# Performance work log

Hardware: AMD Instinct MI355X
Metric: run time of the kernel (lower is better)

Reference implementation:

```python
import jax, jax.numpy as jnp
import numpy as np

B, S, DM = 2, 2048, 1024
H, HD = 16, 64          # n_heads, head_dim
TPF = 128               # tokens_per_frame
NF = S // TPF           # n_frames
EPS = 1e-6
ROPE_THETA = 10000.0
NEG = -1e30  # stand-in for -inf that stays finite under softmax


def setup_inputs() -> dict:
    key = jax.random.key(0)
    ks = jax.random.split(key, 3)
    x = jax.random.normal(ks[0], (B, S, DM), dtype=jnp.float32)
    Wqkv = jax.random.normal(ks[1], (3 * DM, DM), dtype=jnp.float32) * (DM ** -0.5)
    bqkv = jnp.zeros((3 * DM,), dtype=jnp.float32)
    Wout = jax.random.normal(ks[2], (DM, DM), dtype=jnp.float32) * (DM ** -0.5)
    bout = jnp.zeros((DM,), dtype=jnp.float32)
    q_scale = jnp.ones((HD,), dtype=jnp.float32)
    k_scale = jnp.ones((HD,), dtype=jnp.float32)
    return {"x": x, "Wqkv": Wqkv, "bqkv": bqkv, "q_scale": q_scale,
            "k_scale": k_scale, "Wout": Wout, "bout": bout}


def _block_causal_mask(dtype):
    # Frame-block causal: query in frame i may attend keys in frames <= i.
    # Quirk from source: rows of the LAST frame additionally mask frame 0.
    fr = jnp.arange(S) // TPF
    allowed = fr[None, :] <= fr[:, None]
    quirk = (fr[:, None] == NF - 1) & (fr[None, :] == 0)
    allowed = allowed & ~quirk
    return jnp.where(allowed, jnp.zeros((), dtype), jnp.full((), NEG, dtype))


def _rmsnorm(t, scale):
    return t * jax.lax.rsqrt(jnp.mean(t * t, axis=-1, keepdims=True) + EPS) * scale


def _rope(t):
    # half-split rotary over flat token index; t: [B,H,S,D]
    pos = jnp.arange(S, dtype=jnp.float32)
    inv_freq = 1.0 / (ROPE_THETA ** (jnp.arange(0, HD, 2, dtype=jnp.float32) / HD))
    ang = pos[:, None] * inv_freq[None, :]              # [S, D/2]
    cos = jnp.concatenate([jnp.cos(ang), jnp.cos(ang)], axis=-1)  # [S, D]
    sin = jnp.concatenate([jnp.sin(ang), jnp.sin(ang)], axis=-1)
    t1, t2 = jnp.split(t, 2, axis=-1)
    rot = jnp.concatenate([-t2, t1], axis=-1)
    return t * cos + rot * sin


def reference(x, Wqkv, bqkv, q_scale, k_scale, Wout, bout):
    qkv = x @ Wqkv.T + bqkv                        # [B,S,3*DM]
    qkv = qkv.reshape(B, S, 3, H, HD)
    q, k, v = jnp.moveaxis(qkv, 2, 0)              # each [B,S,H,D]
    q = jnp.transpose(q, (0, 2, 1, 3))             # [B,H,S,D]
    k = jnp.transpose(k, (0, 2, 1, 3))
    v = jnp.transpose(v, (0, 2, 1, 3))
    q = _rmsnorm(q, q_scale)
    k = _rmsnorm(k, k_scale)
    q = _rope(q)
    k = _rope(k)
    mask = _block_causal_mask(x.dtype)             # [S,S]
    scores = jnp.einsum('bhqd,bhkd->bhqk', q, k) * (HD ** -0.5) + mask
    attn = jax.nn.softmax(scores, axis=-1)
    o = jnp.einsum('bhqk,bhkd->bhqd', attn, v)     # [B,H,S,D]
    o = jnp.transpose(o, (0, 2, 1, 3)).reshape(B, S, DM)
    return o @ Wout.T + bout
```

## Files before the change

kernel.cpp:

```cpp
#include <hip/hip_runtime.h>
#include <cstddef>
#include <cstdint>

constexpr int CB  = 2;
constexpr int CS  = 2048;
constexpr int CDM = 1024;
constexpr int CH  = 16;
constexpr int CHD = 64;
constexpr int CTPF = 128;
constexpr int CNF = 16;

typedef __attribute__((ext_vector_type(8))) short short8;
typedef __attribute__((ext_vector_type(4))) float f32x4;

__device__ inline ushort f32_bf16_rne(float x) {
  uint32_t u = __float_as_uint(x);
  u += 0x7FFFu + ((u >> 16) & 1u);
  return (ushort)(u >> 16);
}
__device__ inline float bf16_f32(ushort h) {
  return __uint_as_float(((uint32_t)h) << 16);
}
__device__ inline void split8(const float* v, short8& H, short8& L) {
#pragma unroll
  for (int j = 0; j < 8; ++j) {
    const ushort hh = f32_bf16_rne(v[j]);
    H[j] = (short)hh;
    L[j] = (short)f32_bf16_rne(v[j] - bf16_f32(hh));
  }
}

__global__ __launch_bounds__(256) void split3(
    const float* __restrict__ s0, ushort* __restrict__ h0,
    ushort* __restrict__ l0, int n0,
    const float* __restrict__ s1, ushort* __restrict__ h1,
    ushort* __restrict__ l1, int n1,
    const float* __restrict__ s2, ushort* __restrict__ h2,
    ushort* __restrict__ l2, int n2) {
  const int ntot = n0 + n1 + n2;
  int i = blockIdx.x * 256 + threadIdx.x;
  const int stride = gridDim.x * 256;
  for (; i < ntot; i += stride) {
    const float* src;
    ushort *h, *l;
    int j = i;
    if (j < n0) {
      src = s0; h = h0; l = l0;
    } else if ((j -= n0) < n1) {
      src = s1; h = h1; l = l1;
    } else {
      j -= n1; src = s2; h = h2; l = l2;
    }
    float v[8];
    *(float4*)&v[0] = ((const float4*)src)[2 * j];
    *(float4*)&v[4] = ((const float4*)src)[2 * j + 1];
    short8 H, L;
    split8(v, H, L);
    *(short8*)&h[(size_t)j * 8] = H;
    *(short8*)&l[(size_t)j * 8] = L;
  }
}

__global__ __launch_bounds__(256) void gemm_ps(
    const ushort* __restrict__ Ah, const ushort* __restrict__ Al,
    const ushort* __restrict__ Bh, const ushort* __restrict__ Bl,
    const float* __restrict__ bias, float* __restrict__ C,
    int M, int N, int K) {
  __shared__ ushort As_h[128 * 32], As_l[128 * 32];
  __shared__ ushort Bs_h[128 * 32], Bs_l[128 * 32];
  const int tid = threadIdx.x;
  const int bm = blockIdx.y * 128;
  const int bn = blockIdx.x * 128;
  const int wid = tid >> 6;
  const int lane = tid & 63;
  const int wm = wid >> 1;
  const int wn = wid & 1;
  const int l15 = lane & 15;
  const int lk = lane >> 4;
  const int srow = tid >> 2;
  const int kq = (tid & 3) * 8;

  f32x4 acc[4][4];
#pragma unroll
  for (int i = 0; i < 4; ++i)
#pragma unroll
    for (int j = 0; j < 4; ++j) acc[i][j] = (f32x4){0.f, 0.f, 0.f, 0.f};

  for (int k0 = 0; k0 < K; k0 += 32) {
    __syncthreads();
#pragma unroll
    for (int c = 0; c < 2; ++c) {
      const int row = srow + c * 64;
      const int kg = kq ^ ((row & 6) << 2);
      const size_t ga = (size_t)(bm + row) * K + k0 + kg;
      const size_t gb = (size_t)(bn + row) * K + k0 + kg;
      const int lo = tid * 8 + c * 2048;
      __builtin_amdgcn_global_load_lds(
          (const __attribute__((address_space(1))) void*)(Ah + ga),
          (__attribute__((address_space(3))) void*)&As_h[lo], 16, 0, 0);
      __builtin_amdgcn_global_load_lds(
          (const __attribute__((address_space(1))) void*)(Al + ga),
          (__attribute__((address_space(3))) void*)&As_l[lo], 16, 0, 0);
      __builtin_amdgcn_global_load_lds(
          (const __attribute__((address_space(1))) void*)(Bh + gb),
          (__attribute__((address_space(3))) void*)&Bs_h[lo], 16, 0, 0);
      __builtin_amdgcn_global_load_lds(
          (const __attribute__((address_space(1))) void*)(Bl + gb),
          (__attribute__((address_space(3))) void*)&Bs_l[lo], 16, 0, 0);
    }
    __syncthreads();

    short8 ah[4], al[4], bh[4], bl[4];
#pragma unroll
    for (int fI = 0; fI < 4; ++fI) {
      const int ar = wm * 64 + fI * 16 + l15;
      const int aoff = ar * 32 + ((lk * 8) ^ ((ar & 6) << 2));
      ah[fI] = *(const short8*)&As_h[aoff];
      al[fI] = *(const short8*)&As_l[aoff];
      const int br = wn * 64 + fI * 16 + l15;
      const int boff = br * 32 + ((lk * 8) ^ ((br & 6) << 2));
      bh[fI] = *(const short8*)&Bs_h[boff];
      bl[fI] = *(const short8*)&Bs_l[boff];
    }
#pragma unroll
    for (int mf = 0; mf < 4; ++mf)
#pragma unroll
      for (int nf = 0; nf < 4; ++nf) {
        acc[mf][nf] = __builtin_amdgcn_mfma_f32_16x16x32_bf16(
            ah[mf], bh[nf], acc[mf][nf], 0, 0, 0);
        acc[mf][nf] = __builtin_amdgcn_mfma_f32_16x16x32_bf16(
            ah[mf], bl[nf], acc[mf][nf], 0, 0, 0);
        acc[mf][nf] = __builtin_amdgcn_mfma_f32_16x16x32_bf16(
            al[mf], bh[nf], acc[mf][nf], 0, 0, 0);
      }
  }

#pragma unroll
  for (int mf = 0; mf < 4; ++mf)
#pragma unroll
    for (int nf = 0; nf < 4; ++nf) {
      const int col = bn + wn * 64 + nf * 16 + l15;
      const int row0 = bm + wm * 64 + mf * 16 + lk * 4;
      const float bc = bias[col];
#pragma unroll
      for (int i = 0; i < 4; ++i)
        C[(size_t)(row0 + i) * N + col] = acc[mf][nf][i] + bc;
    }
}

__global__ __launch_bounds__(256) void qkv_prep(
    const float* __restrict__ qkv, const float* __restrict__ q_scale,
    const float* __restrict__ k_scale,
    ushort* __restrict__ Qh, ushort* __restrict__ Ql,
    ushort* __restrict__ Kh, ushort* __restrict__ Kl,
    ushort* __restrict__ Vth, ushort* __restrict__ Vtl) {
  __shared__ float Vtile[64][68];
  const int lane = threadIdx.x & 63;
  const int w = threadIdx.x >> 6;
  const int st = blockIdx.x;
  const int h = blockIdx.y;
  const int b = blockIdx.z;

  const float qs = q_scale[lane];
  const float ks = k_scale[lane];
  const int j = lane & 31;
  const float inv = powf(10000.0f, -(float)j * (1.0f / 32.0f));
  const float sgn = (lane < 32) ? -1.f : 1.f;

  for (int it = 0; it < 16; ++it) {
    const int sl = w * 16 + it;
    const int s = st * 64 + sl;
    const size_t row =
        ((size_t)(b * CS + s)) * (3 * CDM) + (size_t)h * CHD + lane;
    float qv = qkv[row];
    float kv = qkv[row + CDM];
    const float vv = qkv[row + 2 * CDM];

    float sq = qv * qv, sk2 = kv * kv;
#pragma unroll
    for (int off = 32; off > 0; off >>= 1) {
      sq += __shfl_xor(sq, off);
      sk2 += __shfl_xor(sk2, off);
    }
    qv *= rsqrtf(sq * (1.f / CHD) + 1e-6f) * qs;
    kv *= rsqrtf(sk2 * (1.f / CHD) + 1e-6f) * ks;

    const float ang = (float)s * inv;
    const float cs = cosf(ang);
    const float sn = sinf(ang);
    const float qp = __shfl_xor(qv, 32);
    const float kp = __shfl_xor(kv, 32);
    const float qr = fmaf(qv, cs, sgn * qp * sn) * 0.125f;
    const float kr = fmaf(kv, cs, sgn * kp * sn);

    const size_t ob = (((size_t)(b * CH + h)) * CS + s) * CHD + lane;
    const ushort qhh = f32_bf16_rne(qr);
    Qh[ob] = qhh;
    Ql[ob] = f32_bf16_rne(qr - bf16_f32(qhh));
    const ushort khh = f32_bf16_rne(kr);
    Kh[ob] = khh;
    Kl[ob] = f32_bf16_rne(kr - bf16_f32(khh));
    Vtile[lane][sl] = vv;
  }
  __syncthreads();
  const int d = threadIdx.x >> 2;
  const int sq4 = (threadIdx.x & 3) * 16;
  const size_t vb = (((size_t)(b * CH + h)) * CHD + d) * CS + st * 64 + sq4;
#pragma unroll
  for (int j0 = 0; j0 < 16; j0 += 8) {
    float v8[8];
#pragma unroll
    for (int jj = 0; jj < 8; ++jj) v8[jj] = Vtile[d][sq4 + j0 + jj];
    short8 H, L;
    split8(v8, H, L);
    *(short8*)&Vth[vb + j0] = H;
    *(short8*)&Vtl[vb + j0] = L;
  }
}

__global__ __launch_bounds__(256, 2) void attn_fwd_mfma(
    const ushort* __restrict__ Qh, const ushort* __restrict__ Ql,
    const ushort* __restrict__ Kh, const ushort* __restrict__ Kl,
    const ushort* __restrict__ Vth, const ushort* __restrict__ Vtl,
    ushort* __restrict__ Oh, ushort* __restrict__ Ol) {
  __shared__ ushort Ks_h[64 * 64], Ks_l[64 * 64];
  __shared__ ushort Vs_h[64 * 64], Vs_l[64 * 64];
  __shared__ ushort Ps_h[128 * 64], Ps_l[128 * 64];
  const int tid = threadIdx.x;
  const int b = blockIdx.x;
  const int h = blockIdx.y;
  const int fsel = blockIdx.z;
  const int f = (fsel < 8) ? (15 - fsel) : (fsel - 8);
  const int lane = tid & 63;
  const int wid = tid >> 6;
  const int l15 = lane & 15;
  const int lk = lane >> 4;
  const int qb = wid * 32;
  const size_t hb = ((size_t)(b * CH + h)) * CS * CHD;
  const size_t vtb = ((size_t)(b * CH + h)) * CHD * CS;

  short8 qh[2][2], ql[2][2];
#pragma unroll
  for (int nf = 0; nf < 2; ++nf)
#pragma unroll
    for (int ks = 0; ks < 2; ++ks) {
      const size_t qoff = hb +
          (size_t)(f * CTPF + qb + nf * 16 + l15) * CHD + ks * 32 + lk * 8;
      qh[nf][ks] = *(const short8*)(Qh + qoff);
      ql[nf][ks] = *(const short8*)(Ql + qoff);
    }

  f32x4 accO[2][4];
#pragma unroll
  for (int mo = 0; mo < 2; ++mo)
#pragma unroll
    for (int no = 0; no < 4; ++no) accO[mo][no] = (f32x4){0.f, 0.f, 0.f, 0.f};
  float m[2] = {-1e30f, -1e30f};
  float lsum[2] = {0.f, 0.f};

  const int kf0 = (f == CNF - 1) ? 1 : 0;
  for (int kf = kf0; kf <= f; ++kf) {
#pragma unroll 1
    for (int half = 0; half < 2; ++half) {
      const int cb = kf * CTPF + half * 64;
      __syncthreads();
      {
        const int r = tid >> 2;
        const int cq = (tid & 3) * 16;
        const int mk = (r & 7) << 3;
        const size_t ko = hb + (size_t)(cb + r) * CHD + cq;
        *(short8*)&Ks_h[r * 64 + (cq ^ mk)] = *(const short8*)(Kh + ko);
        *(short8*)&Ks_h[r * 64 + ((cq + 8) ^ mk)] = *(const short8*)(Kh + ko + 8);
        *(short8*)&Ks_l[r * 64 + (cq ^ mk)] = *(const short8*)(Kl + ko);
        *(short8*)&Ks_l[r * 64 + ((cq + 8) ^ mk)] = *(const short8*)(Kl + ko + 8);
        const size_t vo = vtb + (size_t)r * CS + cb + cq;
        *(short8*)&Vs_h[r * 64 + (cq ^ mk)] = *(const short8*)(Vth + vo);
        *(short8*)&Vs_h[r * 64 + ((cq + 8) ^ mk)] = *(const short8*)(Vth + vo + 8);
        *(short8*)&Vs_l[r * 64 + (cq ^ mk)] = *(const short8*)(Vtl + vo);
        *(short8*)&Vs_l[r * 64 + ((cq + 8) ^ mk)] = *(const short8*)(Vtl + vo + 8);
      }
      __syncthreads();

      f32x4 sacc[4][2];
#pragma unroll
      for (int mf = 0; mf < 4; ++mf)
#pragma unroll
        for (int nf = 0; nf < 2; ++nf) sacc[mf][nf] = (f32x4){0.f, 0.f, 0.f, 0.f};
#pragma unroll
      for (int ks = 0; ks < 2; ++ks) {
        short8 kh[4], kl[4];
#pragma unroll
        for (int mf = 0; mf < 4; ++mf) {
          const int krow = mf * 16 + l15;
          const int base = krow * 64 + ((ks * 32 + lk * 8) ^ ((krow & 7) << 3));
          kh[mf] = *(const short8*)&Ks_h[base];
          kl[mf] = *(const short8*)&Ks_l[base];
        }
#pragma unroll
        for (int mf = 0; mf < 4; ++mf)
#pragma unroll
          for (int nf = 0; nf < 2; ++nf) {
            sacc[mf][nf] = __builtin_amdgcn_mfma_f32_16x16x32_bf16(
                kh[mf], qh[nf][ks], sacc[mf][nf], 0, 0, 0);
            sacc[mf][nf] = __builtin_amdgcn_mfma_f32_16x16x32_bf16(
                kh[mf], ql[nf][ks], sacc[mf][nf], 0, 0, 0);
            sacc[mf][nf] = __builtin_amdgcn_mfma_f32_16x16x32_bf16(
                kl[mf], qh[nf][ks], sacc[mf][nf], 0, 0, 0);
          }
      }

      float c[2];
#pragma unroll
      for (int nf = 0; nf < 2; ++nf) {
        float cm = sacc[0][nf][0];
#pragma unroll
        for (int mf = 0; mf < 4; ++mf)
#pragma unroll
          for (int i = 0; i < 4; ++i) cm = fmaxf(cm, sacc[mf][nf][i]);
        cm = fmaxf(cm, __shfl_xor(cm, 16));
        cm = fmaxf(cm, __shfl_xor(cm, 32));
        const float mn = fmaxf(m[nf], cm);
        c[nf] = __expf(m[nf] - mn);
        m[nf] = mn;
        float ps = 0.f;
        const int qrow = qb + nf * 16 + l15;
        const int qmk = (qrow & 7) << 3;
#pragma unroll
        for (int mf = 0; mf < 4; ++mf) {
          float p0 = __expf(sacc[mf][nf][0] - mn);
          float p1 = __expf(sacc[mf][nf][1] - mn);
          float p2 = __expf(sacc[mf][nf][2] - mn);
          float p3 = __expf(sacc[mf][nf][3] - mn);
          ps += (p0 + p1) + (p2 + p3);
          const ushort h0 = f32_bf16_rne(p0), h1 = f32_bf16_rne(p1);
          const ushort h2 = f32_bf16_rne(p2), h3 = f32_bf16_rne(p3);
          uint2 hw, lw;
          hw.x = (uint32_t)h0 | ((uint32_t)h1 << 16);
          hw.y = (uint32_t)h2 | ((uint32_t)h3 << 16);
          lw.x = (uint32_t)f32_bf16_rne(p0 - bf16_f32(h0)) |
                 ((uint32_t)f32_bf16_rne(p1 - bf16_f32(h1)) << 16);
          lw.y = (uint32_t)f32_bf16_rne(p2 - bf16_f32(h2)) |
                 ((uint32_t)f32_bf16_rne(p3 - bf16_f32(h3)) << 16);
          const int off = qrow * 64 + ((mf * 16 + lk * 4) ^ qmk);
          *(uint2*)&Ps_h[off] = hw;
          *(uint2*)&Ps_l[off] = lw;
        }
        ps += __shfl_xor(ps, 16);
        ps += __shfl_xor(ps, 32);
        lsum[nf] = lsum[nf] * c[nf] + ps;
      }
#pragma unroll
      for (int mo = 0; mo < 2; ++mo)
#pragma unroll
        for (int i = 0; i < 4; ++i) {
          const float cq = __shfl(c[mo], lk * 4 + i);
#pragma unroll
          for (int no = 0; no < 4; ++no) accO[mo][no][i] *= cq;
        }

#pragma unroll
      for (int ks = 0; ks < 2; ++ks) {
        short8 pa_h[2], pa_l[2], vb_h[4], vb_l[4];
#pragma unroll
        for (int mo = 0; mo < 2; ++mo) {
          const int qrow = qb + mo * 16 + l15;
          const int base = qrow * 64 + ((ks * 32 + lk * 8) ^ ((qrow & 7) << 3));
          pa_h[mo] = *(const short8*)&Ps_h[base];
          pa_l[mo] = *(const short8*)&Ps_l[base];
        }
#pragma unroll
        for (int no = 0; no < 4; ++no) {
          const int vrow = no * 16 + l15;
          const int base = vrow * 64 + ((ks * 32 + lk * 8) ^ ((vrow & 7) << 3));
          vb_h[no] = *(const short8*)&Vs_h[base];
          vb_l[no] = *(const short8*)&Vs_l[base];
        }
#pragma unroll
        for (int mo = 0; mo < 2; ++mo)
#pragma unroll
          for (int no = 0; no < 4; ++no) {
            accO[mo][no] = __builtin_amdgcn_mfma_f32_16x16x32_bf16(
                pa_h[mo], vb_h[no], accO[mo][no], 0, 0, 0);
            accO[mo][no] = __builtin_amdgcn_mfma_f32_16x16x32_bf16(
                pa_h[mo], vb_l[no], accO[mo][no], 0, 0, 0);
            accO[mo][no] = __builtin_amdgcn_mfma_f32_16x16x32_bf16(
                pa_l[mo], vb_h[no], accO[mo][no], 0, 0, 0);
          }
      }
    }
  }

  const float il0 = 1.f / lsum[0];
  const float il1 = 1.f / lsum[1];
#pragma unroll
  for (int mo = 0; mo < 2; ++mo) {
    const float myil = (mo == 0) ? il0 : il1;
#pragma unroll
    for (int i = 0; i < 4; ++i) {
      const float wv = __shfl(myil, lk * 4 + i);
      const int srow = f * CTPF + qb + mo * 16 + lk * 4 + i;
      const size_t obase = (size_t)(b * CS + srow) * CDM + h * CHD;
#pragma unroll
      for (int no = 0; no < 4; ++no) {
        const float val = accO[mo][no][i] * wv;
        const ushort hh = f32_bf16_rne(val);
        Oh[obase + no * 16 + l15] = hh;
        Ol[obase + no * 16 + l15] = f32_bf16_rne(val - bf16_f32(hh));
      }
    }
  }
}

extern "C" void kernel_launch(void* const* d_in, const int* in_sizes, int n_in,
                              void* d_out, int out_size, void* d_ws, size_t ws_size,
                              hipStream_t stream) {
  const float* x       = (const float*)d_in[0];
  const float* Wqkv    = (const float*)d_in[1];
  const float* bqkv    = (const float*)d_in[2];
  const float* q_scale = (const float*)d_in[3];
  const float* k_scale = (const float*)d_in[4];
  const float* Wout    = (const float*)d_in[5];
  const float* bout    = (const float*)d_in[6];
  float* out = (float*)d_out;

  ushort* W = (ushort*)d_ws;
  const size_t qkvN = (size_t)(CB * CS) * (3 * CDM);
  const size_t perA = (size_t)CB * CH * CS * CHD;
  const size_t WqN  = (size_t)(3 * CDM) * CDM;
  const size_t WoN  = (size_t)CDM * CDM;

  float*  qkvF = (float*)W;
  ushort* Oh   = W;
  ushort* Ol   = W + perA;
  ushort* R1   = W + 2 * qkvN;
  ushort* Qh = R1;            ushort* Ql = R1 + perA;
  ushort* Kh = R1 + 2 * perA; ushort* Kl = R1 + 3 * perA;
  ushort* Vth = R1 + 4 * perA; ushort* Vtl = R1 + 5 * perA;
  ushort* xh  = R1;            ushort* xl  = R1 + perA;
  ushort* Wqh = R1 + 2 * perA; ushort* Wql = Wqh + WqN;
  ushort* Wouth = R1 + 6 * perA; ushort* Woutl = Wouth + WoN;

  split3<<<2048, 256, 0, stream>>>(x, xh, xl, (int)(perA / 8),
                                   Wqkv, Wqh, Wql, (int)(WqN / 8),
                                   Wout, Wouth, Woutl, (int)(WoN / 8));

  dim3 g1((3 * CDM) / 128, (CB * CS) / 128);
  gemm_ps<<<g1, 256, 0, stream>>>(xh, xl, Wqh, Wql, bqkv, qkvF,
                                  CB * CS, 3 * CDM, CDM);

  dim3 g2(CS / 64, CH, CB);
  qkv_prep<<<g2, 256, 0, stream>>>(qkvF, q_scale, k_scale,
                                   Qh, Ql, Kh, Kl, Vth, Vtl);

  dim3 g3(CB, CH, CNF);
  attn_fwd_mfma<<<g3, 256, 0, stream>>>(Qh, Ql, Kh, Kl, Vth, Vtl, Oh, Ol);

  dim3 g4(CDM / 128, (CB * CS) / 128);
  gemm_ps<<<g4, 256, 0, stream>>>(Oh, Ol, Wouth, Woutl, bout, out,
                                  CB * CS, CDM, CDM);
}
```

Baseline: 252.3 us.

## Pre-swizzle K/V in global memory and load tiles via direct global-to-LDS

The XOR bank-conflict swizzle for K and transposed V is now applied when qkv_prep writes them to global memory. The attention kernel can then copy contiguous tiles straight into shared memory with global_load_lds, skipping the round trip through registers. Separately, the RoPE cos/sin values are precomputed into a table by a new small kernel, so qkv_prep no longer evaluates powf, sinf and cosf per element. The cost is an extra kernel launch, extra workspace for the table, and a global layout that depends on the swizzle.

```diff
diff --git a/kernel.cpp b/kernel.cpp
--- a/kernel.cpp
+++ b/kernel.cpp
@@ -28,6 +28,15 @@
     H[j] = (short)hh;
     L[j] = (short)f32_bf16_rne(v[j] - bf16_f32(hh));
   }
+}
+
+__global__ __launch_bounds__(256) void rope_tab(float2* __restrict__ T) {
+  const int idx = blockIdx.x * 256 + threadIdx.x;
+  const int s = idx >> 5;
+  const int j = idx & 31;
+  const float inv = powf(10000.0f, -(float)j * (1.0f / 32.0f));
+  const float ang = (float)s * inv;
+  T[idx] = make_float2(cosf(ang), sinf(ang));
 }
 
 __global__ __launch_bounds__(256) void split3(
@@ -150,7 +159,7 @@
 
 __global__ __launch_bounds__(256) void qkv_prep(
     const float* __restrict__ qkv, const float* __restrict__ q_scale,
-    const float* __restrict__ k_scale,
+    const float* __restrict__ k_scale, const float2* __restrict__ Trig,
     ushort* __restrict__ Qh, ushort* __restrict__ Ql,
     ushort* __restrict__ Kh, ushort* __restrict__ Kl,
     ushort* __restrict__ Vth, ushort* __restrict__ Vtl) {
@@ -164,7 +173,6 @@
   const float qs = q_scale[lane];
   const float ks = k_scale[lane];
   const int j = lane & 31;
-  const float inv = powf(10000.0f, -(float)j * (1.0f / 32.0f));
   const float sgn = (lane < 32) ? -1.f : 1.f;
 
   for (int it = 0; it < 16; ++it) {
@@ -185,27 +193,30 @@
     qv *= rsqrtf(sq * (1.f / CHD) + 1e-6f) * qs;
     kv *= rsqrtf(sk2 * (1.f / CHD) + 1e-6f) * ks;
 
-    const float ang = (float)s * inv;
-    const float cs = cosf(ang);
-    const float sn = sinf(ang);
+    const float2 cstab = Trig[s * 32 + j];
+    const float cs = cstab.x;
+    const float sn = cstab.y;
     const float qp = __shfl_xor(qv, 32);
     const float kp = __shfl_xor(kv, 32);
     const float qr = fmaf(qv, cs, sgn * qp * sn) * 0.125f;
     const float kr = fmaf(kv, cs, sgn * kp * sn);
 
-    const size_t ob = (((size_t)(b * CH + h)) * CS + s) * CHD + lane;
+    const size_t tok = ((size_t)(b * CH + h)) * CS + s;
+    const size_t obq = tok * CHD + lane;
     const ushort qhh = f32_bf16_rne(qr);
-    Qh[ob] = qhh;
-    Ql[ob] = f32_bf16_rne(qr - bf16_f32(qhh));
+    Qh[obq] = qhh;
+    Ql[obq] = f32_bf16_rne(qr - bf16_f32(qhh));
+    const size_t obk = tok * CHD + (lane ^ ((s & 7) << 3));
     const ushort khh = f32_bf16_rne(kr);
-    Kh[ob] = khh;
-    Kl[ob] = f32_bf16_rne(kr - bf16_f32(khh));
+    Kh[obk] = khh;
+    Kl[obk] = f32_bf16_rne(kr - bf16_f32(khh));
     Vtile[lane][sl] = vv;
   }
   __syncthreads();
   const int d = threadIdx.x >> 2;
   const int sq4 = (threadIdx.x & 3) * 16;
-  const size_t vb = (((size_t)(b * CH + h)) * CHD + d) * CS + st * 64 + sq4;
+  const size_t vrow = (((size_t)(b * CH + h)) * CHD + d) * CS + st * 64;
+  const int vmk = (d & 7) << 3;
 #pragma unroll
   for (int j0 = 0; j0 < 16; j0 += 8) {
     float v8[8];
@@ -213,8 +224,9 @@
     for (int jj = 0; jj < 8; ++jj) v8[jj] = Vtile[d][sq4 + j0 + jj];
     short8 H, L;
     split8(v8, H, L);
-    *(short8*)&Vth[vb + j0] = H;
-    *(short8*)&Vtl[vb + j0] = L;
+    const int c0 = (sq4 + j0) ^ vmk;
+    *(short8*)&Vth[vrow + c0] = H;
+    *(short8*)&Vtl[vrow + c0] = L;
   }
 }
 
@@ -265,19 +277,24 @@
       const int cb = kf * CTPF + half * 64;
       __syncthreads();
       {
-        const int r = tid >> 2;
-        const int cq = (tid & 3) * 16;
-        const int mk = (r & 7) << 3;
-        const size_t ko = hb + (size_t)(cb + r) * CHD + cq;
-        *(short8*)&Ks_h[r * 64 + (cq ^ mk)] = *(const short8*)(Kh + ko);
-        *(short8*)&Ks_h[r * 64 + ((cq + 8) ^ mk)] = *(const short8*)(Kh + ko + 8);
-        *(short8*)&Ks_l[r * 64 + (cq ^ mk)] = *(const short8*)(Kl + ko);
-        *(short8*)&Ks_l[r * 64 + ((cq + 8) ^ mk)] = *(const short8*)(Kl + ko + 8);
-        const size_t vo = vtb + (size_t)r * CS + cb + cq;
-        *(short8*)&Vs_h[r * 64 + (cq ^ mk)] = *(const short8*)(Vth + vo);
-        *(short8*)&Vs_h[r * 64 + ((cq + 8) ^ mk)] = *(const short8*)(Vth + vo + 8);
-        *(short8*)&Vs_l[r * 64 + (cq ^ mk)] = *(const short8*)(Vtl + vo);
-        *(short8*)&Vs_l[r * 64 + ((cq + 8) ^ mk)] = *(const short8*)(Vtl + vo + 8);
+        const size_t kc = hb + (size_t)cb * CHD;
+#pragma unroll
+        for (int q = 0; q < 2; ++q) {
+          const int u = tid * 8 + q * 2048;
+          __builtin_amdgcn_global_load_lds(
+              (const __attribute__((address_space(1))) void*)(Kh + kc + u),
+              (__attribute__((address_space(3))) void*)&Ks_h[u], 16, 0, 0);
+          __builtin_amdgcn_global_load_lds(
+              (const __attribute__((address_space(1))) void*)(Kl + kc + u),
+              (__attribute__((address_space(3))) void*)&Ks_l[u], 16, 0, 0);
+          const size_t va = vtb + (size_t)(u >> 6) * CS + cb + (u & 63);
+          __builtin_amdgcn_global_load_lds(
+              (const __attribute__((address_space(1))) void*)(Vth + va),
+              (__attribute__((address_space(3))) void*)&Vs_h[u], 16, 0, 0);
+          __builtin_amdgcn_global_load_lds(
+              (const __attribute__((address_space(1))) void*)(Vtl + va),
+              (__attribute__((address_space(3))) void*)&Vs_l[u], 16, 0, 0);
+        }
       }
       __syncthreads();
 
@@ -439,7 +456,9 @@
   ushort* xh  = R1;            ushort* xl  = R1 + perA;
   ushort* Wqh = R1 + 2 * perA; ushort* Wql = Wqh + WqN;
   ushort* Wouth = R1 + 6 * perA; ushort* Woutl = Wouth + WoN;
-
+  float2* Trig = (float2*)(Woutl + WoN);
+
+  rope_tab<<<256, 256, 0, stream>>>(Trig);
   split3<<<2048, 256, 0, stream>>>(x, xh, xl, (int)(perA / 8),
                                    Wqkv, Wqh, Wql, (int)(WqN / 8),
                                    Wout, Wouth, Woutl, (int)(WoN / 8));
@@ -449,7 +468,7 @@
                                   CB * CS, 3 * CDM, CDM);
 
   dim3 g2(CS / 64, CH, CB);
-  qkv_prep<<<g2, 256, 0, stream>>>(qkvF, q_scale, k_scale,
+  qkv_prep<<<g2, 256, 0, stream>>>(qkvF, q_scale, k_scale, Trig,
                                    Qh, Ql, Kh, Kl, Vth, Vtl);
 
   dim3 g3(CB, CH, CNF);
```

Measured after the change: 254.1 us. About the same (+0.7%).
